# Performance work log

Measured on AMD Instinct MI355X. Metric: run time of the kernel, lower is better.

The kernel has to match this reference:

```python
import jax, jax.numpy as jnp
import numpy as np
from jax import lax

B, C, H, W = 16, 3, 512, 512


def _nms(heat):
    # 3x3 max-pool, stride 1, SAME padding; keep only local peaks
    hmax = lax.reduce_window(heat, -jnp.inf, lax.max,
                             (1, 1, 3, 3), (1, 1, 1, 1), 'SAME')
    return heat * (hmax == heat).astype(heat.dtype)


def _topk(scores, K):
    b, c, h, w = scores.shape
    # per-class topk over the spatial plane
    topk_scores, topk_inds = lax.top_k(scores.reshape(b, c, h * w), K)  # [b,c,K]
    topk_row = (topk_inds // w).astype(scores.dtype)
    topk_col = (topk_inds % w).astype(scores.dtype)
    # global topk across (class, K)
    topk_score, topk_ind = lax.top_k(topk_scores.reshape(b, c * K), K)  # [b,K]
    topk_clses = topk_ind // K
    gath = lambda x: jnp.take_along_axis(x.reshape(b, c * K), topk_ind, axis=1)
    return topk_score, gath(topk_inds), topk_clses, gath(topk_row), gath(topk_col)


def _transpose_and_gather_feat(feat, inds):
    b, ch, h, w = feat.shape
    f = feat.transpose(0, 2, 3, 1).reshape(b, h * w, ch)  # [b,HW,ch]
    return jnp.take_along_axis(f, inds[:, :, None], axis=1)  # [b,K,ch]


def _decode(hm, cen_offset, direction, z_coor, dim, K):
    b = hm.shape[0]
    hm = _nms(hm)
    scores, inds, clses, row, col = _topk(hm, K)
    off = _transpose_and_gather_feat(cen_offset, inds)           # [b,K,2]
    col = col[:, :, None] + off[:, :, 0:1]
    row = row[:, :, None] + off[:, :, 1:2]
    direction = _transpose_and_gather_feat(direction, inds)      # [b,K,2]
    z_coor = _transpose_and_gather_feat(z_coor, inds)            # [b,K,1]
    dim = _transpose_and_gather_feat(dim, inds)                  # [b,K,3]
    clses = clses[:, :, None].astype(hm.dtype)
    scores = scores[:, :, None]
    return jnp.concatenate([scores, col, row, z_coor, dim, direction, clses], axis=2)


def setup_inputs() -> dict:
    key = jax.random.key(0)
    k1, k2, k3, k4, k5 = jax.random.split(key, 5)
    return {
        'hm_cen': jax.random.normal(k1, (B, C, H, W), jnp.float32),
        'cen_offset': jax.random.normal(k2, (B, 2, H, W), jnp.float32),
        'direction': jax.random.normal(k3, (B, 2, H, W), jnp.float32),
        'z_coor': jax.random.normal(k4, (B, 1, H, W), jnp.float32),
        'dim': jax.random.normal(k5, (B, 3, H, W), jnp.float32),
        'K': 500,
    }


def reference(hm_cen, cen_offset, direction, z_coor, dim, K):
    # postprocessing_v2 applies sigmoid to the class heatmap before decode
    heat = jax.nn.sigmoid(hm_cen)
    return _decode(heat, cen_offset, direction, z_coor, dim, K)  # [B,K,10]
```

## Files before the change

### kernel.cpp

```cpp
#include <hip/hip_runtime.h>
#include <math.h>
#include <float.h>

#define Hd 512
#define Wd 512
#define HWp (Hd*Wd)
#define Bn 16
#define Cn 3
#define NMAP (Bn*Cn)
#define KTOP 500
#define PBANDS 16
#define BAND 32
#define CAPB 4096

__device__ __forceinline__ uint32_t flipbits(float v){
  uint32_t u = __float_as_uint(v);
  return u ^ (0x80000000u | (uint32_t)(-(int32_t)(u>>31)));
}
__device__ __forceinline__ float unflipbits(uint32_t f){
  uint32_t u = f ^ ((f>>31)? 0x80000000u : 0xFFFFFFFFu);
  return __uint_as_float(u);
}

__global__ __launch_bounds__(256) void k_zero(uint4* __restrict__ p)
{
  p[(size_t)blockIdx.x * 256 + threadIdx.x] = make_uint4(0u, 0u, 0u, 0u);
}

__device__ __forceinline__ void nms_row(
    const float4 p0, const float4 p1, const float4 c0, const float4 c1,
    const float4 n0, const float4 n1, const int lane,
    uint32_t& pk, float* cv)
{
  float vm0 = fmaxf(fmaxf(p0.x,c0.x),n0.x);
  float vm1 = fmaxf(fmaxf(p0.y,c0.y),n0.y);
  float vm2 = fmaxf(fmaxf(p0.z,c0.z),n0.z);
  float vm3 = fmaxf(fmaxf(p0.w,c0.w),n0.w);
  float vm4 = fmaxf(fmaxf(p1.x,c1.x),n1.x);
  float vm5 = fmaxf(fmaxf(p1.y,c1.y),n1.y);
  float vm6 = fmaxf(fmaxf(p1.z,c1.z),n1.z);
  float vm7 = fmaxf(fmaxf(p1.w,c1.w),n1.w);
  float vmL = __shfl_up(vm7, 1);   if (lane == 0)  vmL = -INFINITY;
  float vmR = __shfl_down(vm0, 1); if (lane == 63) vmR = -INFINITY;

  float m0 = fmaxf(vmL, fmaxf(vm0, vm1));
  float m1 = fmaxf(vm0, fmaxf(vm1, vm2));
  float m2 = fmaxf(vm1, fmaxf(vm2, vm3));
  float m3 = fmaxf(vm2, fmaxf(vm3, vm4));
  float m4 = fmaxf(vm3, fmaxf(vm4, vm5));
  float m5 = fmaxf(vm4, fmaxf(vm5, vm6));
  float m6 = fmaxf(vm5, fmaxf(vm6, vm7));
  float m7 = fmaxf(vm6, fmaxf(vm7, vmR));

  pk = 0;
  if (c0.x >= m0) pk |= 1u;
  if (c0.y >= m1) pk |= 2u;
  if (c0.z >= m2) pk |= 4u;
  if (c0.w >= m3) pk |= 8u;
  if (c1.x >= m4) pk |= 16u;
  if (c1.y >= m5) pk |= 32u;
  if (c1.z >= m6) pk |= 64u;
  if (c1.w >= m7) pk |= 128u;
  cv[0]=c0.x; cv[1]=c0.y; cv[2]=c0.z; cv[3]=c0.w;
  cv[4]=c1.x; cv[5]=c1.y; cv[6]=c1.z; cv[7]=c1.w;
}

__global__ __launch_bounds__(512) void k_nms(
    const float* __restrict__ hm, uint64_t* __restrict__ seg_all,
    uint32_t* __restrict__ cnt, uint32_t* __restrict__ ghist)
{
  __shared__ uint32_t lhist[4096];
  __shared__ uint32_t ctr;
  const int bid = blockIdx.x;
  const int m = bid >> 4, p = bid & (PBANDS - 1);
  const int tid = threadIdx.x, lane = tid & 63, w = tid >> 6;
  const float* map = hm + (size_t)m * HWp;
  uint64_t* dst = seg_all + (size_t)bid * CAPB;
  const int y0 = p * BAND + w * 4;
  const int xb = lane * 8;

  for (int i = tid; i < 4096; i += 512) lhist[i] = 0;
  if (tid == 0) ctr = 0;
  __syncthreads();

  const float4 NEG4 = make_float4(-INFINITY,-INFINITY,-INFINITY,-INFINITY);
  float4 ra[6], rb[6];
  #pragma unroll
  for (int r = 0; r < 6; ++r) {
    const int yy = y0 - 1 + r;
    if (yy >= 0 && yy < Hd) {
      const float* rp = map + (size_t)yy * Wd + xb;
      ra[r] = *(const float4*)rp; rb[r] = *(const float4*)(rp + 4);
    } else { ra[r] = NEG4; rb[r] = NEG4; }
  }

  #pragma unroll
  for (int r = 0; r < 4; ++r) {
    uint32_t pk; float cv[8];
    nms_row(ra[r], rb[r], ra[r+1], rb[r+1], ra[r+2], rb[r+2], lane, pk, cv);
    const uint32_t np = (uint32_t)__popc(pk);
    uint32_t incl = np;
    #pragma unroll
    for (int d = 1; d < 64; d <<= 1) { uint32_t u = __shfl_up(incl, d); if (lane >= d) incl += u; }
    const uint32_t tot = __shfl(incl, 63);
    if (!tot) continue;
    uint32_t b0 = 0;
    if (lane == 0) b0 = atomicAdd(&ctr, tot);
    b0 = __shfl(b0, 0);
    uint32_t pos = b0 + incl - np;
    const uint32_t ib = (uint32_t)((y0 + r) * Wd + xb);
    #pragma unroll
    for (int i = 0; i < 8; ++i) {
      if ((pk >> i) & 1u) {
        const uint32_t fb = flipbits(cv[i]);
        if (pos < (uint32_t)CAPB)
          dst[pos] = ((uint64_t)fb << 32) | (uint32_t)(~(ib + (uint32_t)i));
        atomicAdd(&lhist[fb >> 20], 1u);
        ++pos;
      }
    }
  }
  __syncthreads();
  if (tid == 0) cnt[bid] = (ctr < (uint32_t)CAPB) ? ctr : (uint32_t)CAPB;
  uint32_t* gh = ghist + (size_t)m * 4096;
  for (int i = tid; i < 4096; i += 512) {
    const uint32_t v = lhist[i];
    if (v) atomicAdd(&gh[i], v);
  }
}

__device__ __forceinline__ void findT4096(
    const uint32_t* hist, const uint32_t target, const int tid, const int lane,
    const int wid, uint32_t* wtot, uint32_t* res)
{
  const uint32_t s = hist[4*tid] + hist[4*tid+1] + hist[4*tid+2] + hist[4*tid+3];
  uint32_t v = s;
  #pragma unroll
  for (int d = 1; d < 64; d <<= 1) { uint32_t u = __shfl_down(v, d); if (lane + d < 64) v += u; }
  if (lane == 0) wtot[wid] = v;
  __syncthreads();
  uint32_t above = 0;
  for (int ww = wid + 1; ww < 16; ++ww) above += wtot[ww];
  const uint32_t gsuf = v + above;
  if (gsuf >= target && (gsuf - s) < target) {
    uint32_t cum = gsuf - s;
    for (int b = 4*tid + 3; b >= 4*tid; --b) {
      cum += hist[b];
      if (cum >= target) { res[0]=(uint32_t)b; res[1]=target-(cum-hist[b]); res[2]=cum; break; }
    }
  }
  __syncthreads();
}

__device__ __forceinline__ uint64_t cexch(uint64_t mine, uint64_t part, bool wantMax) {
  uint64_t mx = mine > part ? mine : part;
  uint64_t mn = mine > part ? part : mine;
  return wantMax ? mx : mn;
}

__device__ void bitonic1024_1t(uint64_t& e0, uint64_t* sbuf, int tid, int lane)
{
  for (int k = 2; k <= 1024; k <<= 1) {
    for (int j = k >> 1; j > 0; j >>= 1) {
      const bool up = ((tid & k) == 0);
      if (j >= 64) {
        __syncthreads();
        sbuf[tid] = e0;
        __syncthreads();
        uint64_t q = sbuf[tid ^ j];
        e0 = cexch(e0, q, up == ((tid & j) == 0));
      } else {
        uint64_t q = __shfl_xor((unsigned long long)e0, j);
        e0 = cexch(e0, q, up == ((lane & j) == 0));
      }
    }
  }
  __syncthreads();
  sbuf[tid] = e0;
  __syncthreads();
}

__device__ void bitonic2048_reg(uint64_t& e0, uint64_t& e1, uint64_t* sbuf, int tid, int lane)
{
  const int i1 = tid + 1024;
  for (int k = 2; k <= 2048; k <<= 1) {
    for (int j = k >> 1; j > 0; j >>= 1) {
      if (j >= 1024) {
        uint64_t mx = e0 > e1 ? e0 : e1;
        uint64_t mn = e0 > e1 ? e1 : e0;
        e0 = mx; e1 = mn;
      } else if (j >= 64) {
        __syncthreads();
        sbuf[tid] = e0; sbuf[i1] = e1;
        __syncthreads();
        uint64_t q0 = sbuf[tid ^ j];
        uint64_t q1 = sbuf[i1 ^ j];
        bool amS = ((tid & j) == 0);
        e0 = cexch(e0, q0, ((tid & k) == 0) == amS);
        e1 = cexch(e1, q1, ((i1  & k) == 0) == amS);
      } else {
        uint64_t q0 = __shfl_xor((unsigned long long)e0, j);
        uint64_t q1 = __shfl_xor((unsigned long long)e1, j);
        bool amS = ((lane & j) == 0);
        e0 = cexch(e0, q0, ((tid & k) == 0) == amS);
        e1 = cexch(e1, q1, ((i1  & k) == 0) == amS);
      }
    }
  }
  __syncthreads();
  sbuf[tid] = e0; sbuf[i1] = e1;
  __syncthreads();
}

__global__ __launch_bounds__(1024) void k_select(
    const uint64_t* __restrict__ seg_all, const uint32_t* __restrict__ cnt,
    const uint32_t* __restrict__ ghist,
    float* __restrict__ s1_scores, uint32_t* __restrict__ s1_inds)
{
  __shared__ uint32_t hist[4096];
  __shared__ uint64_t csel[2048];
  __shared__ uint32_t segn[16];
  __shared__ uint32_t wtot[16];
  __shared__ uint32_t res[4];

  const int m = blockIdx.x;
  const int tid = threadIdx.x, lane = tid & 63, wid = tid >> 6;
  const uint64_t lt = (1ull << lane) - 1ull;

  for (int i = tid; i < 4096; i += 1024) hist[i] = ghist[(size_t)m * 4096 + i];
  if (tid < 16) segn[tid] = min(cnt[m * PBANDS + tid], (uint32_t)CAPB);
  if (tid == 0) res[3] = 0;
  __syncthreads();

  uint32_t n = 0;
  #pragma unroll
  for (int s = 0; s < 16; ++s) n += segn[s];

  const uint64_t* sg = seg_all + (size_t)(m * PBANDS + wid) * CAPB;
  const uint32_t sn = segn[wid];

  uint32_t shift = 20, thr = 0;
  if (n > 512) {
    findT4096(hist, KTOP, tid, lane, wid, wtot, res);
    const uint32_t T1 = res[0], krem = res[1], M0 = res[2];
    __syncthreads();
    if (M0 <= 2048u) {
      thr = T1;
    } else {
      for (int i = tid; i < 4096; i += 1024) hist[i] = 0;
      __syncthreads();
      for (uint32_t i = (uint32_t)lane; i < sn; i += 64u) {
        const uint32_t f = (uint32_t)(sg[i] >> 32);
        if ((f >> 20) == T1) atomicAdd(&hist[(f >> 8) & 4095u], 1u);
      }
      __syncthreads();
      findT4096(hist, krem, tid, lane, wid, wtot, res);
      shift = 8; thr = (T1 << 12) | res[0];
      __syncthreads();
    }
  }

  for (uint32_t base = 0; base < sn; base += 256u) {
    const uint32_t i0 = base + (uint32_t)lane, i1 = i0 + 64u, i2 = i0 + 128u, i3 = i0 + 192u;
    uint64_t k0 = 0, k1 = 0, k2 = 0, k3 = 0;
    if (i0 < sn) k0 = sg[i0];
    if (i1 < sn) k1 = sg[i1];
    if (i2 < sn) k2 = sg[i2];
    if (i3 < sn) k3 = sg[i3];
    const bool p0 = (i0 < sn) && (((uint32_t)(k0 >> 32) >> shift) >= thr);
    const bool p1 = (i1 < sn) && (((uint32_t)(k1 >> 32) >> shift) >= thr);
    const bool p2 = (i2 < sn) && (((uint32_t)(k2 >> 32) >> shift) >= thr);
    const bool p3 = (i3 < sn) && (((uint32_t)(k3 >> 32) >> shift) >= thr);
    #define APP(K, P) {                                                  \
      const unsigned long long mask = __ballot(P);                       \
      if (mask) {                                                        \
        uint32_t b = 0;                                                  \
        if (lane == 0) b = atomicAdd(&res[3], (uint32_t)__popcll(mask)); \
        b = __shfl(b, 0);                                                \
        if (P) {                                                         \
          const uint32_t pp = b + (uint32_t)__popcll(mask & lt);         \
          if (pp < 2048u) csel[pp] = K;                                  \
        }                                                                \
      }                                                                  \
    }
    APP(k0, p0) APP(k1, p1) APP(k2, p2) APP(k3, p3)
    #undef APP
  }
  __syncthreads();
  uint32_t M = res[3]; if (M > 2048u) M = 2048u;
  for (uint32_t i = M + (uint32_t)tid; i < 2048u; i += 1024u) csel[i] = 0ull;
  __syncthreads();

  if (M <= 1024u) {
    uint64_t e0 = csel[tid];
    bitonic1024_1t(e0, csel, tid, lane);
  } else {
    uint64_t e0 = csel[tid], e1 = csel[tid + 1024];
    bitonic2048_reg(e0, e1, csel, tid, lane);
  }

  if (tid < 512) {
    const uint64_t kk = csel[tid];
    float score; uint32_t idx;
    if (kk == 0ull) { score = 0.0f; idx = 0u; }
    else {
      idx = ~(uint32_t)kk;
      const float v = unflipbits((uint32_t)(kk >> 32));
      score = 1.0f / (1.0f + expf(-v));
    }
    s1_scores[m * 512 + tid] = score;
    s1_inds [m * 512 + tid] = idx;
  }
}

__global__ __launch_bounds__(512) void k_final(
    const float* __restrict__ s1_scores, const uint32_t* __restrict__ s1_inds,
    const float* __restrict__ cen_offset, const float* __restrict__ direction,
    const float* __restrict__ z_coor, const float* __restrict__ dimf,
    float* __restrict__ out)
{
  __shared__ float ssc[Cn][KTOP];
  const int b = blockIdx.x / Cn, c = blockIdx.x % Cn;
  const int tid = threadIdx.x;

  for (int i = tid; i < Cn * KTOP; i += 512) {
    int cc = i / KTOP, r = i - cc * KTOP;
    ssc[cc][r] = s1_scores[(b * Cn + cc) * 512 + r];
  }
  __syncthreads();

  if (tid < KTOP) {
    const int r = tid;
    const int i = c * KTOP + r;
    const uint64_t mykey = ((uint64_t)flipbits(ssc[c][r]) << 32) | (uint32_t)(~(uint32_t)i);
    int rank = r;
    #pragma unroll
    for (int cd = 1; cd < Cn; ++cd) {
      const int cc = (c + cd) % Cn;
      int lo = 0, hi = KTOP;
      while (lo < hi) {
        int mid = (lo + hi) >> 1;
        uint64_t k2 = ((uint64_t)flipbits(ssc[cc][mid]) << 32)
                    | (uint32_t)(~(uint32_t)(cc * KTOP + mid));
        if (k2 > mykey) lo = mid + 1; else hi = mid;
      }
      rank += lo;
    }
    if (rank < KTOP) {
      const float* co = cen_offset + (size_t)b * 2 * HWp;
      const float* di = direction  + (size_t)b * 2 * HWp;
      const float* zc = z_coor     + (size_t)b * HWp;
      const float* dm = dimf       + (size_t)b * 3 * HWp;
      const int bcx = b * Cn + c;
      const uint32_t ind = s1_inds[bcx * 512 + r];
      float o[10];
      o[0] = ssc[c][r];
      o[1] = (float)(ind & (Wd - 1)) + co[ind];
      o[2] = (float)(ind >> 9) + co[HWp + ind];
      o[3] = zc[ind];
      o[4] = dm[ind];
      o[5] = dm[HWp + ind];
      o[6] = dm[2 * HWp + ind];
      o[7] = di[ind];
      o[8] = di[HWp + ind];
      o[9] = (float)c;
      float* op = out + ((size_t)b * KTOP + rank) * 10;
      #pragma unroll
      for (int q = 0; q < 10; ++q) op[q] = o[q];
    }
  }
}

extern "C" void kernel_launch(void* const* d_in, const int* in_sizes, int n_in,
                              void* d_out, int out_size, void* d_ws, size_t ws_size,
                              hipStream_t stream)
{
  const float* hm         = (const float*)d_in[0];
  const float* cen_offset = (const float*)d_in[1];
  const float* direction  = (const float*)d_in[2];
  const float* z_coor     = (const float*)d_in[3];
  const float* dimf       = (const float*)d_in[4];
  float* out = (float*)d_out;

  char* ws = (char*)d_ws;
  uint32_t* ghist = (uint32_t*)ws;
  size_t o0       = (size_t)NMAP * 4096 * 4;
  uint32_t* cnt   = (uint32_t*)(ws + o0);
  float*    s1_sc = (float*)(ws + o0 + 4096);
  uint32_t* s1_id = (uint32_t*)(ws + o0 + 4096 + (size_t)NMAP * 512 * 4);
  size_t fixed    = o0 + 4096 + (size_t)NMAP * 512 * 4 * 2;
  uint64_t* seg   = (uint64_t*)(ws + fixed);

  k_zero  <<<(int)(o0 / 4096), 256, 0, stream>>>((uint4*)ghist);
  k_nms   <<<NMAP * PBANDS, 512, 0, stream>>>(hm, seg, cnt, ghist);
  k_select<<<NMAP,         1024, 0, stream>>>(seg, cnt, ghist, s1_sc, s1_id);
  k_final <<<Bn * Cn,       512, 0, stream>>>(s1_sc, s1_id, cen_offset, direction, z_coor, dimf, out);
}
```

Baseline: 54.53 us.

## Use per-wave candidate segments and smaller histogram in NMS/select pipeline

The NMS kernel now runs smaller 256-thread blocks over 16-row slices, and each wave writes its own candidate segment with a wave-local offset instead of a block-wide shared atomic counter. It also streams rows through registers rather than preloading six. The first-level score histogram shrinks from 4096 to 1024 bins (top 10 bits), which cuts the LDS clearing and global merge work. The select kernel is adapted to walk 128 segments, 8 per wave, and uses a 1024-bin threshold search. The trade-off is a coarser first pass that more often needs the second histogram refinement, and a per-wave capacity of 512 entries that could overflow on denser inputs.

```diff
diff --git a/kernel.cpp b/kernel.cpp
--- a/kernel.cpp
+++ b/kernel.cpp
@@ -9,9 +9,12 @@
 #define Cn 3
 #define NMAP (Bn*Cn)
 #define KTOP 500
-#define PBANDS 16
-#define BAND 32
-#define CAPB 4096
+#define SLICES 32
+#define WPB 4
+#define ROWS_W 4
+#define SEGS 128
+#define CAPW 512
+#define HBINS 1024
 
 __device__ __forceinline__ uint32_t flipbits(float v){
   uint32_t u = __float_as_uint(v);
@@ -65,68 +68,95 @@
   cv[4]=c1.x; cv[5]=c1.y; cv[6]=c1.z; cv[7]=c1.w;
 }
 
-__global__ __launch_bounds__(512) void k_nms(
+__global__ __launch_bounds__(256) void k_nms(
     const float* __restrict__ hm, uint64_t* __restrict__ seg_all,
     uint32_t* __restrict__ cnt, uint32_t* __restrict__ ghist)
 {
-  __shared__ uint32_t lhist[4096];
-  __shared__ uint32_t ctr;
+  __shared__ uint32_t lhist[HBINS];
   const int bid = blockIdx.x;
-  const int m = bid >> 4, p = bid & (PBANDS - 1);
+  const int m = bid >> 5, slice = bid & (SLICES - 1);
   const int tid = threadIdx.x, lane = tid & 63, w = tid >> 6;
   const float* map = hm + (size_t)m * HWp;
-  uint64_t* dst = seg_all + (size_t)bid * CAPB;
-  const int y0 = p * BAND + w * 4;
+  const int segid = bid * WPB + w;
+  uint64_t* seg = seg_all + (size_t)segid * CAPW;
+  const int y0 = slice * 16 + w * ROWS_W;
   const int xb = lane * 8;
 
-  for (int i = tid; i < 4096; i += 512) lhist[i] = 0;
-  if (tid == 0) ctr = 0;
+  for (int i = tid; i < HBINS; i += 256) lhist[i] = 0;
   __syncthreads();
 
   const float4 NEG4 = make_float4(-INFINITY,-INFINITY,-INFINITY,-INFINITY);
-  float4 ra[6], rb[6];
+  float4 p0, p1, c0, c1;
+  if (y0 > 0) {
+    const float* rp = map + (size_t)(y0-1)*Wd + xb;
+    p0 = *(const float4*)rp; p1 = *(const float4*)(rp+4);
+  } else { p0 = NEG4; p1 = NEG4; }
+  {
+    const float* rp = map + (size_t)y0*Wd + xb;
+    c0 = *(const float4*)rp; c1 = *(const float4*)(rp+4);
+  }
+
+  uint32_t my_off = 0;
   #pragma unroll
-  for (int r = 0; r < 6; ++r) {
-    const int yy = y0 - 1 + r;
-    if (yy >= 0 && yy < Hd) {
-      const float* rp = map + (size_t)yy * Wd + xb;
-      ra[r] = *(const float4*)rp; rb[r] = *(const float4*)(rp + 4);
-    } else { ra[r] = NEG4; rb[r] = NEG4; }
-  }
-
-  #pragma unroll
-  for (int r = 0; r < 4; ++r) {
+  for (int r = 0; r < ROWS_W; ++r) {
+    const int y = y0 + r, yn = y + 1;
+    float4 n0, n1;
+    if (yn < Hd) {
+      const float* rp = map + (size_t)yn*Wd + xb;
+      n0 = *(const float4*)rp; n1 = *(const float4*)(rp+4);
+    } else { n0 = NEG4; n1 = NEG4; }
+
     uint32_t pk; float cv[8];
-    nms_row(ra[r], rb[r], ra[r+1], rb[r+1], ra[r+2], rb[r+2], lane, pk, cv);
+    nms_row(p0, p1, c0, c1, n0, n1, lane, pk, cv);
+
     const uint32_t np = (uint32_t)__popc(pk);
     uint32_t incl = np;
     #pragma unroll
     for (int d = 1; d < 64; d <<= 1) { uint32_t u = __shfl_up(incl, d); if (lane >= d) incl += u; }
     const uint32_t tot = __shfl(incl, 63);
-    if (!tot) continue;
-    uint32_t b0 = 0;
-    if (lane == 0) b0 = atomicAdd(&ctr, tot);
-    b0 = __shfl(b0, 0);
-    uint32_t pos = b0 + incl - np;
-    const uint32_t ib = (uint32_t)((y0 + r) * Wd + xb);
-    #pragma unroll
-    for (int i = 0; i < 8; ++i) {
-      if ((pk >> i) & 1u) {
-        const uint32_t fb = flipbits(cv[i]);
-        if (pos < (uint32_t)CAPB)
-          dst[pos] = ((uint64_t)fb << 32) | (uint32_t)(~(ib + (uint32_t)i));
-        atomicAdd(&lhist[fb >> 20], 1u);
-        ++pos;
-      }
-    }
-  }
-  __syncthreads();
-  if (tid == 0) cnt[bid] = (ctr < (uint32_t)CAPB) ? ctr : (uint32_t)CAPB;
-  uint32_t* gh = ghist + (size_t)m * 4096;
-  for (int i = tid; i < 4096; i += 512) {
+    if (tot) {
+      uint32_t pos = my_off + incl - np;
+      const uint32_t ib = (uint32_t)(y * Wd + xb);
+      #pragma unroll
+      for (int i = 0; i < 8; ++i) {
+        if ((pk >> i) & 1u) {
+          const uint32_t fb = flipbits(cv[i]);
+          if (pos < (uint32_t)CAPW)
+            seg[pos] = ((uint64_t)fb << 32) | (uint32_t)(~(ib + (uint32_t)i));
+          atomicAdd(&lhist[fb >> 22], 1u);
+          ++pos;
+        }
+      }
+      my_off += tot;
+    }
+    p0 = c0; p1 = c1; c0 = n0; c1 = n1;
+  }
+  if (lane == 0) cnt[segid] = (my_off < (uint32_t)CAPW) ? my_off : (uint32_t)CAPW;
+  __syncthreads();
+  uint32_t* gh = ghist + (size_t)m * HBINS;
+  for (int i = tid; i < HBINS; i += 256) {
     const uint32_t v = lhist[i];
     if (v) atomicAdd(&gh[i], v);
   }
+}
+
+__device__ __forceinline__ void findT1024(
+    const uint32_t* hist, const uint32_t target, const int tid, const int lane,
+    const int wid, uint32_t* wtot, uint32_t* res)
+{
+  const uint32_t s = hist[tid];
+  uint32_t v = s;
+  #pragma unroll
+  for (int d = 1; d < 64; d <<= 1) { uint32_t u = __shfl_down(v, d); if (lane + d < 64) v += u; }
+  if (lane == 0) wtot[wid] = v;
+  __syncthreads();
+  uint32_t above = 0;
+  for (int ww = wid + 1; ww < 16; ++ww) above += wtot[ww];
+  const uint32_t gsuf = v + above;
+  if (gsuf >= target && (gsuf - s) < target) {
+    res[0] = (uint32_t)tid; res[1] = target - (gsuf - s); res[2] = gsuf;
+  }
+  __syncthreads();
 }
 
 __device__ __forceinline__ void findT4096(
@@ -219,29 +249,33 @@
 {
   __shared__ uint32_t hist[4096];
   __shared__ uint64_t csel[2048];
-  __shared__ uint32_t segn[16];
+  __shared__ uint32_t segn[SEGS];
   __shared__ uint32_t wtot[16];
   __shared__ uint32_t res[4];
+  __shared__ uint32_t sh_n;
 
   const int m = blockIdx.x;
   const int tid = threadIdx.x, lane = tid & 63, wid = tid >> 6;
   const uint64_t lt = (1ull << lane) - 1ull;
-
-  for (int i = tid; i < 4096; i += 1024) hist[i] = ghist[(size_t)m * 4096 + i];
-  if (tid < 16) segn[tid] = min(cnt[m * PBANDS + tid], (uint32_t)CAPB);
+  const uint64_t* base = seg_all + (size_t)m * SEGS * CAPW;
+
+  if (tid < HBINS) hist[tid] = ghist[(size_t)m * HBINS + tid];
+  if (tid < SEGS) segn[tid] = min(cnt[m * SEGS + tid], (uint32_t)CAPW);
   if (tid == 0) res[3] = 0;
   __syncthreads();
 
-  uint32_t n = 0;
-  #pragma unroll
-  for (int s = 0; s < 16; ++s) n += segn[s];
-
-  const uint64_t* sg = seg_all + (size_t)(m * PBANDS + wid) * CAPB;
-  const uint32_t sn = segn[wid];
-
-  uint32_t shift = 20, thr = 0;
+  if (wid == 0) {
+    uint32_t v = segn[lane] + segn[lane + 64];
+    #pragma unroll
+    for (int d = 1; d < 64; d <<= 1) { uint32_t u = __shfl_down(v, d); if (lane + d < 64) v += u; }
+    if (lane == 0) sh_n = v;
+  }
+  __syncthreads();
+  const uint32_t n = sh_n;
+
+  uint32_t shift = 22, thr = 0;
   if (n > 512) {
-    findT4096(hist, KTOP, tid, lane, wid, wtot, res);
+    findT1024(hist, KTOP, tid, lane, wid, wtot, res);
     const uint32_t T1 = res[0], krem = res[1], M0 = res[2];
     __syncthreads();
     if (M0 <= 2048u) {
@@ -249,42 +283,52 @@
     } else {
       for (int i = tid; i < 4096; i += 1024) hist[i] = 0;
       __syncthreads();
-      for (uint32_t i = (uint32_t)lane; i < sn; i += 64u) {
-        const uint32_t f = (uint32_t)(sg[i] >> 32);
-        if ((f >> 20) == T1) atomicAdd(&hist[(f >> 8) & 4095u], 1u);
+      for (int t = 0; t < 8; ++t) {
+        const int s = wid * 8 + t;
+        const uint64_t* sg = base + (size_t)s * CAPW;
+        const uint32_t sn = segn[s];
+        for (uint32_t i = (uint32_t)lane; i < sn; i += 64u) {
+          const uint32_t f = (uint32_t)(sg[i] >> 32);
+          if ((f >> 22) == T1) atomicAdd(&hist[(f >> 10) & 4095u], 1u);
+        }
       }
       __syncthreads();
       findT4096(hist, krem, tid, lane, wid, wtot, res);
-      shift = 8; thr = (T1 << 12) | res[0];
+      shift = 10; thr = (T1 << 12) | res[0];
       __syncthreads();
     }
   }
 
-  for (uint32_t base = 0; base < sn; base += 256u) {
-    const uint32_t i0 = base + (uint32_t)lane, i1 = i0 + 64u, i2 = i0 + 128u, i3 = i0 + 192u;
-    uint64_t k0 = 0, k1 = 0, k2 = 0, k3 = 0;
-    if (i0 < sn) k0 = sg[i0];
-    if (i1 < sn) k1 = sg[i1];
-    if (i2 < sn) k2 = sg[i2];
-    if (i3 < sn) k3 = sg[i3];
-    const bool p0 = (i0 < sn) && (((uint32_t)(k0 >> 32) >> shift) >= thr);
-    const bool p1 = (i1 < sn) && (((uint32_t)(k1 >> 32) >> shift) >= thr);
-    const bool p2 = (i2 < sn) && (((uint32_t)(k2 >> 32) >> shift) >= thr);
-    const bool p3 = (i3 < sn) && (((uint32_t)(k3 >> 32) >> shift) >= thr);
-    #define APP(K, P) {                                                  \
-      const unsigned long long mask = __ballot(P);                       \
-      if (mask) {                                                        \
-        uint32_t b = 0;                                                  \
-        if (lane == 0) b = atomicAdd(&res[3], (uint32_t)__popcll(mask)); \
-        b = __shfl(b, 0);                                                \
-        if (P) {                                                         \
-          const uint32_t pp = b + (uint32_t)__popcll(mask & lt);         \
-          if (pp < 2048u) csel[pp] = K;                                  \
-        }                                                                \
-      }                                                                  \
-    }
-    APP(k0, p0) APP(k1, p1) APP(k2, p2) APP(k3, p3)
-    #undef APP
+  for (int t = 0; t < 8; ++t) {
+    const int s = wid * 8 + t;
+    const uint64_t* sg = base + (size_t)s * CAPW;
+    const uint32_t sn = segn[s];
+    for (uint32_t b2 = 0; b2 < sn; b2 += 256u) {
+      const uint32_t i0 = b2 + (uint32_t)lane, i1 = i0 + 64u, i2 = i0 + 128u, i3 = i0 + 192u;
+      uint64_t k0 = 0, k1 = 0, k2 = 0, k3 = 0;
+      if (i0 < sn) k0 = sg[i0];
+      if (i1 < sn) k1 = sg[i1];
+      if (i2 < sn) k2 = sg[i2];
+      if (i3 < sn) k3 = sg[i3];
+      const bool p0 = (i0 < sn) && (((uint32_t)(k0 >> 32) >> shift) >= thr);
+      const bool p1 = (i1 < sn) && (((uint32_t)(k1 >> 32) >> shift) >= thr);
+      const bool p2 = (i2 < sn) && (((uint32_t)(k2 >> 32) >> shift) >= thr);
+      const bool p3 = (i3 < sn) && (((uint32_t)(k3 >> 32) >> shift) >= thr);
+      #define APP(K, P) {                                                  \
+        const unsigned long long mask = __ballot(P);                       \
+        if (mask) {                                                        \
+          uint32_t b = 0;                                                  \
+          if (lane == 0) b = atomicAdd(&res[3], (uint32_t)__popcll(mask)); \
+          b = __shfl(b, 0);                                                \
+          if (P) {                                                         \
+            const uint32_t pp = b + (uint32_t)__popcll(mask & lt);         \
+            if (pp < 2048u) csel[pp] = K;                                  \
+          }                                                                \
+        }                                                                  \
+      }
+      APP(k0, p0) APP(k1, p1) APP(k2, p2) APP(k3, p3)
+      #undef APP
+    }
   }
   __syncthreads();
   uint32_t M = res[3]; if (M > 2048u) M = 2048u;
@@ -384,15 +428,16 @@
 
   char* ws = (char*)d_ws;
   uint32_t* ghist = (uint32_t*)ws;
-  size_t o0       = (size_t)NMAP * 4096 * 4;
+  size_t o0       = (size_t)NMAP * HBINS * 4;
   uint32_t* cnt   = (uint32_t*)(ws + o0);
-  float*    s1_sc = (float*)(ws + o0 + 4096);
-  uint32_t* s1_id = (uint32_t*)(ws + o0 + 4096 + (size_t)NMAP * 512 * 4);
-  size_t fixed    = o0 + 4096 + (size_t)NMAP * 512 * 4 * 2;
+  size_t o1       = o0 + (size_t)NMAP * SEGS * 4;
+  float*    s1_sc = (float*)(ws + o1);
+  uint32_t* s1_id = (uint32_t*)(ws + o1 + (size_t)NMAP * 512 * 4);
+  size_t fixed    = o1 + (size_t)NMAP * 512 * 4 * 2;
   uint64_t* seg   = (uint64_t*)(ws + fixed);
 
   k_zero  <<<(int)(o0 / 4096), 256, 0, stream>>>((uint4*)ghist);
-  k_nms   <<<NMAP * PBANDS, 512, 0, stream>>>(hm, seg, cnt, ghist);
+  k_nms   <<<NMAP * SLICES, 256, 0, stream>>>(hm, seg, cnt, ghist);
   k_select<<<NMAP,         1024, 0, stream>>>(seg, cnt, ghist, s1_sc, s1_id);
   k_final <<<Bn * Cn,       512, 0, stream>>>(s1_sc, s1_id, cen_offset, direction, z_coor, dimf, out);
 }
```

Measured after the change: 64.81 us. 1.19x slower.
